# Performance work log

Hardware: AMD Instinct MI355X
Metric: run time of the kernel (lower is better)

The kernel has to match this reference:

```python
import jax, jax.numpy as jnp
import numpy as np

C = 64      # planes_num = prod(discrete_shape)
H = 256     # cont_size[0]
W = 256     # cont_size[1]
L0 = 1024   # len(grid[0])
L1 = 1024   # len(grid[1])
A = -0.75   # bicubic convolution constant (matches PyTorch grid_sample)


def _cubic_weights(t):
    # t: fractional part in [0,1), shape (N,). Weights for taps at offsets -1,0,1,2.
    t2 = t * t
    t3 = t2 * t
    w0 = A * (t3 - 2.0 * t2 + t)                 # cubic_conv2(1+t)
    w1 = (A + 2.0) * t3 - (A + 3.0) * t2 + 1.0   # cubic_conv1(t)
    s = 1.0 - t
    s2 = s * s
    w2 = (A + 2.0) * s2 * s - (A + 3.0) * s2 + 1.0  # cubic_conv1(1-t)
    u = 1.0 + s                                   # = 2 - t
    w3 = A * (u * u * u) - 5.0 * A * (u * u) + 8.0 * A * u - 4.0 * A  # cubic_conv2(2-t)
    return jnp.stack([w0, w1, w2, w3], axis=-1)   # (N,4)


def _prep(g, size):
    # align_corners=True unnormalization: [-1,1] -> [0, size-1]
    x = (g + 1.0) * 0.5 * (size - 1)
    x0 = jnp.floor(x)
    t = x - x0
    idx = x0.astype(jnp.int32)[:, None] + jnp.arange(-1, 3)  # (N,4) tap indices
    idx = jnp.clip(idx, 0, size - 1)                          # padding_mode='border'
    return idx, _cubic_weights(t)


def setup_inputs() -> dict:
    key = jax.random.key(0)
    k1, k2, k3 = jax.random.split(key, 3)
    values = jax.random.uniform(k1, (1, C, H, W), dtype=jnp.float32)  # torch.rand init
    g0 = jax.random.uniform(k2, (L0,), dtype=jnp.float32) * 2.0 - 1.0  # normalized coords
    g1 = jax.random.uniform(k3, (L1,), dtype=jnp.float32) * 2.0 - 1.0
    return {"values": values, "g0": g0, "g1": g1}


def reference(values, g0, g1):
    # preprocess_grid: meshgrid(grid[::-1], 'ij') stacked -> grid[i,j] = (x=g1[i], y=g0[j])
    # grid_sample(values, grid, bicubic, border, align_corners=True)
    v = values[0]                 # (C,H,W)
    xi, wx = _prep(g1, W)         # x taps/weights, (L1,4)
    yi, wy = _prep(g0, H)         # y taps/weights, (L0,4)
    out = jnp.zeros((v.shape[0], g1.shape[0], g0.shape[0]), values.dtype)  # (C,L1,L0)
    for a in range(4):            # 4x4 separable bicubic taps (fixed small loop)
        xa = xi[:, a][:, None]    # (L1,1)
        wa = wx[:, a][:, None]    # (L1,1)
        for b in range(4):
            w = wa * wy[:, b][None, :]                 # (L1,L0)
            out = out + w * v[:, yi[:, b][None, :], xa]  # gather -> (C,L1,L0)
    return out[None]              # (1, C, L1, L0)
```

## Files before the change

### kernel.cpp

```cpp
#include <hip/hip_runtime.h>

#define C_   64
#define H_   256
#define W_   256
#define L0_  1024
#define L1_  1024
#define JT   32
#define ROWP 33
#define HYR  259

__device__ __forceinline__ void cubic_weights(float t, float w[4]) {
    const float A = -0.75f;
    float t2 = t * t, t3 = t2 * t;
    w[0] = A * (t3 - 2.0f * t2 + t);
    w[1] = (A + 2.0f) * t3 - (A + 3.0f) * t2 + 1.0f;
    float s = 1.0f - t, s2 = s * s;
    w[2] = (A + 2.0f) * s2 * s - (A + 3.0f) * s2 + 1.0f;
    float u = 2.0f - t, u2 = u * u;
    w[3] = A * u2 * u - 5.0f * A * u2 + 8.0f * A * u - 4.0f * A;
}

__global__ __launch_bounds__(256, 2) void bicubic_pair(const float* __restrict__ v,
                                                       const float* __restrict__ g0,
                                                       const float* __restrict__ g1,
                                                       float* __restrict__ out) {
    __shared__ float2 hy2[HYR * ROWP];
    __shared__ float2 wAB[L1_];
    __shared__ float  wC [L1_];

    const int t  = threadIdx.x;
    const int c0 = blockIdx.y * 2;
    const int j0 = blockIdx.x * JT;

    {
        const int ib = t * 4;
#pragma unroll
        for (int s = 0; s < 4; ++s) {
            int i = ib + s;
            float x  = (g1[i] + 1.0f) * 0.5f * (float)(W_ - 1);
            float x0 = floorf(x);
            int   ix = min(max((int)x0, 0), W_ - 1);
            float w4[4]; cubic_weights(x - x0, w4);
            wAB[i] = make_float2(w4[0], w4[1]);
            wC[i]  = __uint_as_float((__float_as_uint(w4[2]) & 0xFFFFFF00u)
                                     | (unsigned)ix);
        }
    }

    const int lane = t & 63;
    const int wv   = t >> 6;

    {
        const float* vA = v + (size_t)c0 * (H_ * W_);
        const float* vB = vA + (H_ * W_);
#pragma unroll
        for (int jj = 0; jj < JT / 4; ++jj) {
            int j = wv * (JT / 4) + jj;
            float xg = (g0[j0 + j] + 1.0f) * 0.5f * (float)(H_ - 1);
            float x0 = floorf(xg);
            int   iy = (int)x0;
            float wy[4]; cubic_weights(xg - x0, wy);
            const int y0 = min(max(iy - 1, 0), H_ - 1) * W_;
            const int y1 = min(max(iy,     0), H_ - 1) * W_;
            const int y2 = min(max(iy + 1, 0), H_ - 1) * W_;
            const int y3 = min(max(iy + 2, 0), H_ - 1) * W_;
#pragma unroll
            for (int k = 0; k < 4; ++k) {
                int x_ = lane + 64 * k;
                float a = wy[0] * vA[y0 + x_] + wy[1] * vA[y1 + x_]
                        + wy[2] * vA[y2 + x_] + wy[3] * vA[y3 + x_];
                float b = wy[0] * vB[y0 + x_] + wy[1] * vB[y1 + x_]
                        + wy[2] * vB[y2 + x_] + wy[3] * vB[y3 + x_];
                float2 val = make_float2(a, b);
                hy2[(x_ + 1) * ROWP + j] = val;
                if (x_ == 0)   hy2[j] = val;
                if (x_ == 255) {
                    hy2[257 * ROWP + j] = val;
                    hy2[258 * ROWP + j] = val;
                }
            }
        }
    }
    __syncthreads();

    {
        const int jl    = t & 31;
        const int ihalf = (t >> 5) & 1;
        int i = wv * 256 + ihalf;
        float* o0 = out + (size_t)c0 * ((size_t)L1_ * L0_)
                  + (size_t)i * L0_ + j0 + jl;
        float* o1 = o0 + (size_t)L1_ * L0_;
#pragma unroll 4
        for (int it = 0; it < 128; ++it, i += 2, o0 += 2 * L0_, o1 += 2 * L0_) {
            float2 ab = wAB[i];
            float  cw = wC[i];
            int    ix = (int)(__float_as_uint(cw) & 0xFFu);
            float  w3 = 1.0f - ab.x - ab.y - cw;
            const float2* hp = &hy2[ix * ROWP + jl];
            float2 h0 = hp[0];
            float2 h1 = hp[ROWP];
            float2 h2 = hp[2 * ROWP];
            float2 h3 = hp[3 * ROWP];
            *o0 = ab.x * h0.x + ab.y * h1.x + cw * h2.x + w3 * h3.x;
            *o1 = ab.x * h0.y + ab.y * h1.y + cw * h2.y + w3 * h3.y;
        }
    }
}

extern "C" void kernel_launch(void* const* d_in, const int* in_sizes, int n_in,
                              void* d_out, int out_size, void* d_ws, size_t ws_size,
                              hipStream_t stream) {
    const float* values = (const float*)d_in[0];
    const float* g0     = (const float*)d_in[1];
    const float* g1     = (const float*)d_in[2];
    float* out          = (float*)d_out;

    dim3 grid(L0_ / JT, C_ / 2);
    bicubic_pair<<<grid, 256, 0, stream>>>(values, g0, g1, out);
}
```

Measured before the change: 70.46 us.

## Transpose values into workspace and interpolate along x first with row-contiguous stores

```diff
diff --git a/kernel.cpp b/kernel.cpp
--- a/kernel.cpp
+++ b/kernel.cpp
@@ -5,6 +5,8 @@
 #define W_   256
 #define L0_  1024
 #define L1_  1024
+#define IT   32
+#define HXW  260
 #define JT   32
 #define ROWP 33
 #define HYR  259
@@ -20,6 +22,109 @@
     w[3] = A * u2 * u - 5.0f * A * u2 + 8.0f * A * u - 4.0f * A;
 }
 
+__global__ __launch_bounds__(256) void transpose_v(const float* __restrict__ v,
+                                                   float* __restrict__ vT) {
+    __shared__ float tile[64][65];
+    const int c   = blockIdx.y;
+    const int x0  = (blockIdx.x & 3) * 64;
+    const int y0  = (blockIdx.x >> 2) * 64;
+    const int t   = threadIdx.x;
+    const int lx  = t & 63;
+    const int l4  = t >> 6;
+    const float* vc = v  + (size_t)c * (H_ * W_);
+    float*      vTc = vT + (size_t)c * (H_ * W_);
+#pragma unroll
+    for (int r = 0; r < 16; ++r) {
+        int yl = l4 + 4 * r;
+        tile[yl][lx] = vc[(size_t)(y0 + yl) * W_ + (x0 + lx)];
+    }
+    __syncthreads();
+#pragma unroll
+    for (int r = 0; r < 16; ++r) {
+        int xl = l4 + 4 * r;
+        vTc[(size_t)(x0 + xl) * H_ + (y0 + lx)] = tile[lx][xl];
+    }
+}
+
+__global__ __launch_bounds__(256, 2) void bicubic_xfirst(const float* __restrict__ vT,
+                                                         const float* __restrict__ g0,
+                                                         const float* __restrict__ g1,
+                                                         float* __restrict__ out) {
+    __shared__ float2 hx2[IT * HXW];
+    __shared__ float2 wAB[L0_];
+    __shared__ float  wC [L0_];
+
+    const int t = threadIdx.x;
+    const int bid  = blockIdx.x;
+    const int slot = bid >> 3;
+    const int c0   = ((bid & 7) * 4 + (slot >> 5)) * 2;
+    const int i0   = (slot & 31) * IT;
+
+    {
+        const int jb = t * 4;
+#pragma unroll
+        for (int s = 0; s < 4; ++s) {
+            int j = jb + s;
+            float x  = (g0[j] + 1.0f) * 0.5f * (float)(H_ - 1);
+            float x0 = floorf(x);
+            int   iy = min(max((int)x0, 0), H_ - 1);
+            float w4[4]; cubic_weights(x - x0, w4);
+            wAB[j] = make_float2(w4[0], w4[1]);
+            wC[j]  = __uint_as_float((__float_as_uint(w4[2]) & 0xFFFFFF00u)
+                                     | (unsigned)iy);
+        }
+    }
+
+    {
+        const float* vA = vT + (size_t)c0 * (H_ * W_);
+        const float* vB = vA + (H_ * W_);
+#pragma unroll 4
+        for (int ii = 0; ii < IT; ++ii) {
+            float x  = (g1[i0 + ii] + 1.0f) * 0.5f * (float)(W_ - 1);
+            float x0 = floorf(x);
+            int   ix = (int)x0;
+            float wx[4]; cubic_weights(x - x0, wx);
+            const int r0 = min(max(ix - 1, 0), W_ - 1) * H_;
+            const int r1 = min(max(ix,     0), W_ - 1) * H_;
+            const int r2 = min(max(ix + 1, 0), W_ - 1) * H_;
+            const int r3 = min(max(ix + 2, 0), W_ - 1) * H_;
+            float a = wx[0]*vA[r0+t] + wx[1]*vA[r1+t] + wx[2]*vA[r2+t] + wx[3]*vA[r3+t];
+            float b = wx[0]*vB[r0+t] + wx[1]*vB[r1+t] + wx[2]*vB[r2+t] + wx[3]*vB[r3+t];
+            float2 val = make_float2(a, b);
+            hx2[ii * HXW + (t + 1)] = val;
+            if (t == 0)   hx2[ii * HXW] = val;
+            if (t == 255) { hx2[ii * HXW + 257] = val; hx2[ii * HXW + 258] = val; }
+        }
+    }
+    __syncthreads();
+
+    {
+        float2 ab[4]; float cw[4], w3[4]; int ykb[4];
+#pragma unroll
+        for (int jc = 0; jc < 4; ++jc) {
+            const int j = jc * 256 + t;
+            ab[jc]  = wAB[j];
+            cw[jc]  = wC[j];
+            ykb[jc] = (int)(__float_as_uint(cw[jc]) & 0xFFu);
+            w3[jc]  = 1.0f - ab[jc].x - ab[jc].y - cw[jc];
+        }
+        float* ob0 = out + (size_t)c0 * ((size_t)L1_ * L0_) + (size_t)i0 * L0_;
+        float* ob1 = ob0 + (size_t)L1_ * L0_;
+#pragma unroll 2
+        for (int ii = 0; ii < IT; ++ii) {
+            const float2* hbase = &hx2[ii * HXW];
+#pragma unroll
+            for (int jc = 0; jc < 4; ++jc) {
+                const float2* hp = hbase + ykb[jc];
+                float2 h0 = hp[0], h1 = hp[1], h2 = hp[2], h3 = hp[3];
+                const size_t off = (size_t)ii * L0_ + jc * 256 + t;
+                ob0[off] = ab[jc].x*h0.x + ab[jc].y*h1.x + cw[jc]*h2.x + w3[jc]*h3.x;
+                ob1[off] = ab[jc].x*h0.y + ab[jc].y*h1.y + cw[jc]*h2.y + w3[jc]*h3.y;
+            }
+        }
+    }
+}
+
 __global__ __launch_bounds__(256, 2) void bicubic_pair(const float* __restrict__ v,
                                                        const float* __restrict__ g0,
                                                        const float* __restrict__ g1,
@@ -31,7 +136,6 @@
     const int t  = threadIdx.x;
     const int c0 = blockIdx.y * 2;
     const int j0 = blockIdx.x * JT;
-
     {
         const int ib = t * 4;
 #pragma unroll
@@ -46,10 +150,8 @@
                                      | (unsigned)ix);
         }
     }
-
     const int lane = t & 63;
     const int wv   = t >> 6;
-
     {
         const float* vA = v + (size_t)c0 * (H_ * W_);
         const float* vB = vA + (H_ * W_);
@@ -67,28 +169,21 @@
 #pragma unroll
             for (int k = 0; k < 4; ++k) {
                 int x_ = lane + 64 * k;
-                float a = wy[0] * vA[y0 + x_] + wy[1] * vA[y1 + x_]
-                        + wy[2] * vA[y2 + x_] + wy[3] * vA[y3 + x_];
-                float b = wy[0] * vB[y0 + x_] + wy[1] * vB[y1 + x_]
-                        + wy[2] * vB[y2 + x_] + wy[3] * vB[y3 + x_];
+                float a = wy[0]*vA[y0+x_] + wy[1]*vA[y1+x_] + wy[2]*vA[y2+x_] + wy[3]*vA[y3+x_];
+                float b = wy[0]*vB[y0+x_] + wy[1]*vB[y1+x_] + wy[2]*vB[y2+x_] + wy[3]*vB[y3+x_];
                 float2 val = make_float2(a, b);
                 hy2[(x_ + 1) * ROWP + j] = val;
                 if (x_ == 0)   hy2[j] = val;
-                if (x_ == 255) {
-                    hy2[257 * ROWP + j] = val;
-                    hy2[258 * ROWP + j] = val;
-                }
+                if (x_ == 255) { hy2[257 * ROWP + j] = val; hy2[258 * ROWP + j] = val; }
             }
         }
     }
     __syncthreads();
-
     {
         const int jl    = t & 31;
         const int ihalf = (t >> 5) & 1;
         int i = wv * 256 + ihalf;
-        float* o0 = out + (size_t)c0 * ((size_t)L1_ * L0_)
-                  + (size_t)i * L0_ + j0 + jl;
+        float* o0 = out + (size_t)c0 * ((size_t)L1_ * L0_) + (size_t)i * L0_ + j0 + jl;
         float* o1 = o0 + (size_t)L1_ * L0_;
 #pragma unroll 4
         for (int it = 0; it < 128; ++it, i += 2, o0 += 2 * L0_, o1 += 2 * L0_) {
@@ -101,8 +196,8 @@
             float2 h1 = hp[ROWP];
             float2 h2 = hp[2 * ROWP];
             float2 h3 = hp[3 * ROWP];
-            *o0 = ab.x * h0.x + ab.y * h1.x + cw * h2.x + w3 * h3.x;
-            *o1 = ab.x * h0.y + ab.y * h1.y + cw * h2.y + w3 * h3.y;
+            *o0 = ab.x*h0.x + ab.y*h1.x + cw*h2.x + w3*h3.x;
+            *o1 = ab.x*h0.y + ab.y*h1.y + cw*h2.y + w3*h3.y;
         }
     }
 }
@@ -115,6 +210,12 @@
     const float* g1     = (const float*)d_in[2];
     float* out          = (float*)d_out;
 
-    dim3 grid(L0_ / JT, C_ / 2);
-    bicubic_pair<<<grid, 256, 0, stream>>>(values, g0, g1, out);
-}
+    const size_t vt_bytes = (size_t)C_ * H_ * W_ * 4;
+    if (d_ws && ws_size >= vt_bytes) {
+        float* vT = (float*)d_ws;
+        transpose_v<<<dim3(16, C_), 256, 0, stream>>>(values, vT);
+        bicubic_xfirst<<<dim3(1024), 256, 0, stream>>>(vT, g0, g1, out);
+    } else {
+        bicubic_pair<<<dim3(L0_ / JT, C_ / 2), 256, 0, stream>>>(values, g0, g1, out);
+    }
+}
```

Measured after the change: 83.72 us. 18.8% more time.
